# Kernel optimization log

Measured on AMD Instinct MI355X. Metric: run time of the kernel, lower is better.

## Reference

```python
import jax, jax.numpy as jnp
import numpy as np

# Standard SMPL kinematic tree (child -> parent); root's entry unused.
PARENTS = np.array([0, 0, 0, 0, 1, 2, 3, 4, 5, 6, 7, 8, 9, 9, 9, 12, 13, 14, 16, 17, 18, 19, 20, 21], dtype=np.int32)
N_JOINTS = 24


def _rodrigues(r):
    # r: [..., 3] axis-angle -> [..., 3, 3] rotation matrices.
    # Original adds N(0,1e-8) noise to avoid div-by-zero; we use a deterministic eps.
    theta = jnp.linalg.norm(r, axis=-1, keepdims=True) + 1e-8
    rh = r / theta
    cos = jnp.cos(theta)[..., None]
    sin = jnp.sin(theta)[..., None]
    z = jnp.zeros_like(rh[..., 0])
    K = jnp.stack([z, -rh[..., 2], rh[..., 1],
                   rh[..., 2], z, -rh[..., 0],
                   -rh[..., 1], rh[..., 0], z], axis=-1).reshape(r.shape[:-1] + (3, 3))
    outer = rh[..., :, None] * rh[..., None, :]
    eye = jnp.eye(3, dtype=r.dtype)
    return cos * eye + (1.0 - cos) * outer + sin * K


def setup_inputs() -> dict:
    key = jax.random.key(0)
    ks = jax.random.split(key, 7)
    N, V, J, B = 512, 6890, 24, 10
    beta = jax.random.normal(ks[0], (N, B), dtype=jnp.float32)
    pose = jax.random.normal(ks[1], (N, J * 3), dtype=jnp.float32)
    v_template = jax.random.normal(ks[2], (V, 3), dtype=jnp.float32)
    shapedirs = jax.random.normal(ks[3], (V, 3, B), dtype=jnp.float32) * 0.03
    posedirs = jax.random.normal(ks[4], (V, 3, (J - 1) * 9), dtype=jnp.float32) * 0.01
    J_regressor = jax.random.uniform(ks[5], (J, V), dtype=jnp.float32)
    J_regressor = J_regressor / jnp.sum(J_regressor, axis=1, keepdims=True)  # NonNegUnitSum(axis=1)
    weights = jax.random.uniform(ks[6], (V, J), dtype=jnp.float32)
    weights = weights / jnp.sum(weights, axis=1, keepdims=True)  # NonNegUnitSum(axis=1)
    return {"beta": beta, "pose": pose, "v_template": v_template, "shapedirs": shapedirs,
            "posedirs": posedirs, "J_regressor": J_regressor, "weights": weights}


def reference(beta, pose, v_template, shapedirs, posedirs, J_regressor, weights):
    N = beta.shape[0]
    dt = beta.dtype
    # Shape blendshapes: [N,V,3]
    v_shaped = jnp.einsum('nb,vcb->nvc', beta, shapedirs) + v_template
    # Joint locations: [N,J,3]
    J_loc = jnp.einsum('jv,nvc->njc', J_regressor, v_shaped)
    # Per-joint rotations: [N,24,3,3]
    R = _rodrigues(pose.reshape(N, N_JOINTS, 3))
    # Pose blendshapes
    lrotmin = (R[:, 1:] - jnp.eye(3, dtype=dt)).reshape(N, (N_JOINTS - 1) * 9)
    v_posed = v_shaped + jnp.einsum('np,vcp->nvc', lrotmin, posedirs)
    # Kinematic chain of 4x4 transforms
    bottom = jnp.broadcast_to(jnp.array([0.0, 0.0, 0.0, 1.0], dtype=dt), (N, 1, 4))

    def make_T(Rm, t):  # [N,3,3], [N,3] -> [N,4,4]
        return jnp.concatenate([jnp.concatenate([Rm, t[..., None]], axis=-1), bottom], axis=-2)

    G = [make_T(R[:, 0], J_loc[:, 0])]
    for i in range(1, N_JOINTS):
        p = int(PARENTS[i])
        G.append(jnp.matmul(G[p], make_T(R[:, i], J_loc[:, i] - J_loc[:, p])))
    G = jnp.stack(G, axis=1)  # [N,24,4,4]
    # Remove rest-pose joint translation: G[...,:,3] -= G @ [J,0]
    Jh = jnp.concatenate([J_loc, jnp.zeros_like(J_loc[..., :1])], axis=-1)  # [N,24,4]
    RJ = jnp.einsum('njab,njb->nja', G, Jh)
    G = G - jnp.pad(RJ[..., None], ((0, 0), (0, 0), (0, 0), (3, 0)))
    # Linear blend skinning: per-vertex blended transform [N,V,4,4]
    T = jnp.einsum('njab,vj->nvab', G, weights)
    vh = jnp.concatenate([v_posed, jnp.ones_like(v_posed[..., :1])], axis=-1)  # [N,V,4]
    v = jnp.einsum('nvab,nvb->nva', T, vh)
    return v[..., :3]
```

## Files before the change

### kernel.cpp

```cpp
#include <hip/hip_runtime.h>

#define V_CNT 6890
#define N_B 512
#define NP 207
#define RTOT 20670
#define BPACK_BLKS 1296
#define JS1_BLKS 192
#define W_BLKS 27
#define FUSE_X 108
#define FUSE_BLKS 864

typedef unsigned short ushort_t;
typedef __attribute__((ext_vector_type(4))) float f32x4;
typedef __attribute__((ext_vector_type(8))) short s16x8;
typedef __attribute__((ext_vector_type(4))) short s16x4;

#define O_PART 0u
#define O_G2   65536u
#define O_A    655360u
#define O_W    917504u
#define O_B    1441792u

__device__ __constant__ int PAR[24] = {0,0,0,0,1,2,3,4,5,6,7,8,9,9,9,12,13,14,16,17,18,19,20,21};
__device__ __constant__ int LVL[36] = {
    1, 2, 3,-1,   4, 5, 6,-1,   7, 8, 9,-1,
   10,11,12,13,  14,-1,-1,-1,  15,16,17,-1,
   18,19,-1,-1,  20,21,-1,-1,  22,23,-1,-1};

__device__ __forceinline__ ushort_t f2bf(float f) {
    union { float f; unsigned u; } x; x.f = f;
    unsigned u = x.u + 0x7fffu + ((x.u >> 16) & 1u);
    return (ushort_t)(u >> 16);
}
__device__ __forceinline__ float bf2f(ushort_t h) {
    union { unsigned u; float f; } x; x.u = ((unsigned)h) << 16;
    return x.f;
}

__global__ __launch_bounds__(256) void k_pre(const float* __restrict__ pdirs,
                                             const float* __restrict__ sdirs,
                                             const float* __restrict__ vtemp,
                                             const float* __restrict__ jreg,
                                             const float* __restrict__ wts,
                                             ushort_t* __restrict__ Bswz,
                                             float* __restrict__ part,
                                             ushort_t* __restrict__ Wp) {
    __shared__ float rows[3312];
    __shared__ float red[4][33];
    int b = blockIdx.x;
    int tid = threadIdx.x;
    if (b < BPACK_BLKS) {
        int rtile = b;
        int base = rtile * 16 * NP;
        const int TOTF = RTOT * NP;
        for (int i = tid; i < 16 * NP; i += 256) {
            int gi = base + i;
            rows[i] = (gi < TOTF) ? pdirs[gi] : 0.f;
        }
        __syncthreads();
        for (int c = tid; c < 448; c += 256) {
            int kc = c >> 6, lane = c & 63;
            int quad = lane >> 4, lm = lane & 15;
            int r = rtile * 16 + lm;
            int k0 = kc * 32 + quad * 8;
            bool rv = (r < RTOT);
            s16x8 pk;
#pragma unroll
            for (int i = 0; i < 8; i++) {
                int k = k0 + i;
                float v = 0.f;
                if (rv) {
                    if (k < NP) v = rows[lm * NP + k];
                    else if (k < 217) v = sdirs[(size_t)r * 10 + (k - NP)];
                }
                pk[i] = (short)f2bf(v);
            }
            *(s16x8*)(Bswz + ((size_t)(rtile * 7 + kc) * 64 + lane) * 8) = pk;
        }
    } else if (b < BPACK_BLKS + JS1_BLKS) {
        int b2 = b - BPACK_BLKS;
        int ch = b2 & 7;
        int j = b2 >> 3;
        int v0 = ch * 862;
        int vend = v0 + 862; if (vend > V_CNT) vend = V_CNT;
        float acc[33];
#pragma unroll
        for (int i = 0; i < 33; i++) acc[i] = 0.f;
        for (int v = v0 + tid; v < vend; v += 256) {
            float r = jreg[j * V_CNT + v];
            const float* sd = sdirs + v * 30;
#pragma unroll
            for (int i = 0; i < 30; i++) acc[i] += r * sd[i];
            acc[30] += r * vtemp[v * 3 + 0];
            acc[31] += r * vtemp[v * 3 + 1];
            acc[32] += r * vtemp[v * 3 + 2];
        }
#pragma unroll
        for (int off = 32; off > 0; off >>= 1) {
#pragma unroll
            for (int i = 0; i < 33; i++) acc[i] += __shfl_down(acc[i], off);
        }
        int w = tid >> 6, lane = tid & 63;
        if (lane == 0) {
#pragma unroll
            for (int i = 0; i < 33; i++) red[w][i] = acc[i];
        }
        __syncthreads();
        if (tid < 33) {
            float s = red[0][tid] + red[1][tid] + red[2][tid] + red[3][tid];
            part[b2 * 33 + tid] = s;
        }
    } else {
        int v = (b - BPACK_BLKS - JS1_BLKS) * 256 + tid;
        ushort_t o[32];
        if (v < V_CNT) {
            const float* wr = wts + v * 24;
#pragma unroll
            for (int j = 0; j < 24; j++) o[j] = f2bf(wr[j]);
        } else {
#pragma unroll
            for (int j = 0; j < 24; j++) o[j] = 0;
        }
#pragma unroll
        for (int j = 24; j < 32; j++) o[j] = 0;
#pragma unroll
        for (int q = 0; q < 4; q++)
            *(s16x8*)(Wp + (size_t)v * 32 + q * 8) = *(s16x8*)&o[q * 8];
    }
}

__global__ __launch_bounds__(128) void k_chain(const float* __restrict__ beta,
                                               const float* __restrict__ pose,
                                               const float* __restrict__ part,
                                               ushort_t* __restrict__ G2,
                                               ushort_t* __restrict__ Aswz) {
    __shared__ float JSl[720];
    __shared__ float JTl[72];
    __shared__ float Rl[2][24][9];
    __shared__ float Jl[2][24][3];
    __shared__ float Tm[2][24][16];
    __shared__ float G[2][24][16];
    __shared__ float Gp[2][24][12];
    int tid = threadIdx.x;

    for (int t = tid; t < 792; t += 128) {
        int j = t / 33, i = t - j * 33;
        float s = 0.f;
#pragma unroll
        for (int c = 0; c < 8; c++) s += part[(j * 8 + c) * 33 + i];
        if (i < 30) JSl[j * 30 + i] = s;
        else        JTl[j * 3 + (i - 30)] = s;
    }
    __syncthreads();

    int sub = tid >> 6, lane = tid & 63;
    int n = blockIdx.x * 2 + sub;

    if (lane < 24) {
        int t = lane;
        float x = pose[n * 72 + t * 3 + 0];
        float y = pose[n * 72 + t * 3 + 1];
        float z = pose[n * 72 + t * 3 + 2];
        float th = sqrtf(x * x + y * y + z * z) + 1e-8f;
        float inv = 1.f / th;
        float rx = x * inv, ry = y * inv, rz = z * inv;
        float c = cosf(th), s = sinf(th), omc = 1.f - c;
        Rl[sub][t][0] = c + omc * rx * rx;
        Rl[sub][t][1] = omc * rx * ry - s * rz;
        Rl[sub][t][2] = omc * rx * rz + s * ry;
        Rl[sub][t][3] = omc * ry * rx + s * rz;
        Rl[sub][t][4] = c + omc * ry * ry;
        Rl[sub][t][5] = omc * ry * rz - s * rx;
        Rl[sub][t][6] = omc * rz * rx - s * ry;
        Rl[sub][t][7] = omc * rz * ry + s * rx;
        Rl[sub][t][8] = c + omc * rz * rz;
#pragma unroll
        for (int cc = 0; cc < 3; cc++) {
            float a = JTl[t * 3 + cc];
#pragma unroll
            for (int b = 0; b < 10; b++) a += beta[n * 10 + b] * JSl[(t * 3 + cc) * 10 + b];
            Jl[sub][t][cc] = a;
        }
    }
    __syncthreads();
    if (lane < 24) {
        int t = lane;
        int p = PAR[t];
        float tx, ty, tz;
        if (t == 0) { tx = Jl[sub][0][0]; ty = Jl[sub][0][1]; tz = Jl[sub][0][2]; }
        else { tx = Jl[sub][t][0] - Jl[sub][p][0]; ty = Jl[sub][t][1] - Jl[sub][p][1]; tz = Jl[sub][t][2] - Jl[sub][p][2]; }
        Tm[sub][t][0] = Rl[sub][t][0]; Tm[sub][t][1] = Rl[sub][t][1]; Tm[sub][t][2]  = Rl[sub][t][2]; Tm[sub][t][3]  = tx;
        Tm[sub][t][4] = Rl[sub][t][3]; Tm[sub][t][5] = Rl[sub][t][4]; Tm[sub][t][6]  = Rl[sub][t][5]; Tm[sub][t][7]  = ty;
        Tm[sub][t][8] = Rl[sub][t][6]; Tm[sub][t][9] = Rl[sub][t][7]; Tm[sub][t][10] = Rl[sub][t][8]; Tm[sub][t][11] = tz;
        Tm[sub][t][12] = 0.f; Tm[sub][t][13] = 0.f; Tm[sub][t][14] = 0.f; Tm[sub][t][15] = 1.f;
    }
    __syncthreads();
    if (lane < 16) G[sub][0][lane] = Tm[sub][0][lane];
    __syncthreads();
#pragma unroll
    for (int p9 = 0; p9 < 9; p9++) {
        int slot = lane >> 4, el = lane & 15;
        int j = LVL[p9 * 4 + slot];
        if (j >= 0) {
            int par = PAR[j];
            int a = el >> 2, bb = el & 3;
            float s = G[sub][par][a * 4 + 0] * Tm[sub][j][0 * 4 + bb]
                    + G[sub][par][a * 4 + 1] * Tm[sub][j][1 * 4 + bb]
                    + G[sub][par][a * 4 + 2] * Tm[sub][j][2 * 4 + bb]
                    + G[sub][par][a * 4 + 3] * Tm[sub][j][3 * 4 + bb];
            G[sub][j][el] = s;
        }
        __syncthreads();
    }
    if (lane < 24) {
        int t = lane;
        float jx = Jl[sub][t][0], jy = Jl[sub][t][1], jz = Jl[sub][t][2];
#pragma unroll
        for (int a = 0; a < 3; a++) {
            float g0 = G[sub][t][a * 4 + 0], g1 = G[sub][t][a * 4 + 1];
            float g2 = G[sub][t][a * 4 + 2], g3 = G[sub][t][a * 4 + 3];
            Gp[sub][t][a * 4 + 0] = g0;
            Gp[sub][t][a * 4 + 1] = g1;
            Gp[sub][t][a * 4 + 2] = g2;
            Gp[sub][t][a * 4 + 3] = g3 - (g0 * jx + g1 * jy + g2 * jz);
        }
    }
    __syncthreads();
    {
        int quad = lane >> 4, lm = lane & 15;
        s16x8 pk;
#pragma unroll
        for (int jj = 0; jj < 8; jj++) {
            int joint = quad * 8 + jj;
            float val = (joint < 24 && lm < 12) ? Gp[sub][joint][lm] : 0.f;
            pk[jj] = (short)f2bf(val);
        }
        *(s16x8*)(G2 + (size_t)n * 512 + lane * 8) = pk;
    }
    if (lane < 28) {
        int kc = lane >> 2, quad2 = lane & 3;
        s16x8 pk;
#pragma unroll
        for (int j = 0; j < 8; j++) {
            int k = kc * 32 + quad2 * 8 + j;
            float val;
            if (k < NP) {
                int jo = 1 + k / 9;
                int e = k - (jo - 1) * 9;
                float d = (e == 0 || e == 4 || e == 8) ? 1.f : 0.f;
                val = Rl[sub][jo][e] - d;
            } else if (k < 217) {
                val = beta[n * 10 + (k - NP)];
            } else val = 0.f;
            pk[j] = (short)f2bf(val);
        }
        *(s16x8*)(Aswz + (((size_t)(n >> 4) * 7 + kc) * 64 + (quad2 * 16 + (n & 15))) * 8) = pk;
    }
}

__global__ __launch_bounds__(256) void k_fused(const ushort_t* __restrict__ Aswz,
                                               const ushort_t* __restrict__ Bswz,
                                               const ushort_t* __restrict__ Wp,
                                               const ushort_t* __restrict__ G2,
                                               const float* __restrict__ vtemp,
                                               float* __restrict__ out) {
    __shared__ ushort_t vp[4][96][36];
    int bid = blockIdx.x;
    int tt = (bid & 7) * FUSE_X + (bid >> 3);
    int bx = tt >> 3, by = tt & 7;
    int tid = threadIdx.x, w = tid >> 6, lane = tid & 63;
    int quad = lane >> 4, lm = lane & 15;
    int rh = w & 1, nh = w >> 1;
    int n_w = by * 64 + nh * 32;
    int vs_w = bx * 64 + rh * 32;
    int rtile0 = bx * 12 + rh * 6;
    int ntile0 = by * 4 + nh * 2;

    f32x4 acc[2][6];
#pragma unroll
    for (int a = 0; a < 2; a++)
#pragma unroll
        for (int b = 0; b < 6; b++) acc[a][b] = (f32x4)0.f;

    s16x8 af[2][2], bf[2][6];
#pragma unroll
    for (int mt = 0; mt < 2; mt++)
        af[0][mt] = *(const s16x8*)(Aswz + ((size_t)(ntile0 + mt) * 7 + 0) * 512 + lane * 8);
#pragma unroll
    for (int rt = 0; rt < 6; rt++)
        bf[0][rt] = *(const s16x8*)(Bswz + ((size_t)(rtile0 + rt) * 7 + 0) * 512 + lane * 8);
#pragma unroll
    for (int kc = 0; kc < 7; kc++) {
        int cur = kc & 1, nxt = cur ^ 1;
        if (kc < 6) {
#pragma unroll
            for (int mt = 0; mt < 2; mt++)
                af[nxt][mt] = *(const s16x8*)(Aswz + ((size_t)(ntile0 + mt) * 7 + kc + 1) * 512 + lane * 8);
#pragma unroll
            for (int rt = 0; rt < 6; rt++)
                bf[nxt][rt] = *(const s16x8*)(Bswz + ((size_t)(rtile0 + rt) * 7 + kc + 1) * 512 + lane * 8);
        }
#pragma unroll
        for (int mt = 0; mt < 2; mt++)
#pragma unroll
            for (int rt = 0; rt < 6; rt++)
                acc[mt][rt] = __builtin_amdgcn_mfma_f32_16x16x32_bf16(af[cur][mt], bf[cur][rt], acc[mt][rt], 0, 0, 0);
    }

    float vt[6];
#pragma unroll
    for (int rt = 0; rt < 6; rt++) {
        int col = bx * 192 + rh * 96 + rt * 16 + lm;
        vt[rt] = (col < RTOT) ? vtemp[col] : 0.f;
    }
#pragma unroll
    for (int mt = 0; mt < 2; mt++) {
#pragma unroll
        for (int rt = 0; rt < 6; rt++) {
            int rl = rt * 16 + lm;
            int nl0 = mt * 16 + quad * 4;
            s16x4 pk;
            pk[0] = (short)f2bf(acc[mt][rt][0] + vt[rt]);
            pk[1] = (short)f2bf(acc[mt][rt][1] + vt[rt]);
            pk[2] = (short)f2bf(acc[mt][rt][2] + vt[rt]);
            pk[3] = (short)f2bf(acc[mt][rt][3] + vt[rt]);
            *(s16x4*)&vp[w][rl][nl0] = pk;
        }
    }

    s16x8 wf[2];
#pragma unroll
    for (int mt = 0; mt < 2; mt++)
        wf[mt] = *(const s16x8*)(Wp + (size_t)(vs_w + mt * 16 + lm) * 32 + quad * 8);

    s16x8 ga = *(const s16x8*)(G2 + (size_t)n_w * 512 + lane * 8);
    s16x8 gb = *(const s16x8*)(G2 + (size_t)(n_w + 1) * 512 + lane * 8);
#pragma unroll 1
    for (int t = 0; t < 16; t++) {
        int na = n_w + 2 * t;
        s16x8 gan, gbn;
        if (t < 15) {
            gan = *(const s16x8*)(G2 + (size_t)(na + 2) * 512 + lane * 8);
            gbn = *(const s16x8*)(G2 + (size_t)(na + 3) * 512 + lane * 8);
        }
        f32x4 ta[2], tb[2];
#pragma unroll
        for (int mt = 0; mt < 2; mt++) {
            ta[mt] = __builtin_amdgcn_mfma_f32_16x16x32_bf16(ga, wf[mt], (f32x4)0.f, 0, 0, 0);
            tb[mt] = __builtin_amdgcn_mfma_f32_16x16x32_bf16(gb, wf[mt], (f32x4)0.f, 0, 0, 0);
        }
        if (quad < 3) {
#pragma unroll
            for (int mt = 0; mt < 2; mt++) {
                int v = vs_w + mt * 16 + lm;
                if (v < V_CNT) {
                    int vloc = mt * 16 + lm;
                    unsigned pw0 = *(const unsigned*)&vp[w][vloc * 3 + 0][2 * t];
                    unsigned pw1 = *(const unsigned*)&vp[w][vloc * 3 + 1][2 * t];
                    unsigned pw2 = *(const unsigned*)&vp[w][vloc * 3 + 2][2 * t];
                    float p0a = bf2f((ushort_t)(pw0 & 0xffffu)), p0b = bf2f((ushort_t)(pw0 >> 16));
                    float p1a = bf2f((ushort_t)(pw1 & 0xffffu)), p1b = bf2f((ushort_t)(pw1 >> 16));
                    float p2a = bf2f((ushort_t)(pw2 & 0xffffu)), p2b = bf2f((ushort_t)(pw2 >> 16));
                    float oa = ta[mt][3] + ta[mt][0] * p0a + ta[mt][1] * p1a + ta[mt][2] * p2a;
                    float ob = tb[mt][3] + tb[mt][0] * p0b + tb[mt][1] * p1b + tb[mt][2] * p2b;
                    out[((size_t)na * V_CNT + v) * 3 + quad] = oa;
                    out[((size_t)(na + 1) * V_CNT + v) * 3 + quad] = ob;
                }
            }
        }
        ga = gan; gb = gbn;
    }
}

extern "C" void kernel_launch(void* const* d_in, const int* in_sizes, int n_in,
                              void* d_out, int out_size, void* d_ws, size_t ws_size,
                              hipStream_t stream) {
    const float* beta  = (const float*)d_in[0];
    const float* pose  = (const float*)d_in[1];
    const float* vtemp = (const float*)d_in[2];
    const float* sdirs = (const float*)d_in[3];
    const float* pdirs = (const float*)d_in[4];
    const float* jreg  = (const float*)d_in[5];
    const float* wts   = (const float*)d_in[6];
    char* ws = (char*)d_ws;
    float*    ws_part = (float*)(ws + O_PART);
    ushort_t* ws_G2   = (ushort_t*)(ws + O_G2);
    ushort_t* ws_A    = (ushort_t*)(ws + O_A);
    ushort_t* ws_W    = (ushort_t*)(ws + O_W);
    ushort_t* ws_B    = (ushort_t*)(ws + O_B);
    float* out = (float*)d_out;

    k_pre<<<dim3(BPACK_BLKS + JS1_BLKS + W_BLKS), dim3(256), 0, stream>>>(
        pdirs, sdirs, vtemp, jreg, wts, ws_B, ws_part, ws_W);
    k_chain<<<dim3(N_B / 2), dim3(128), 0, stream>>>(beta, pose, ws_part, ws_G2, ws_A);
    k_fused<<<dim3(FUSE_BLKS), dim3(256), 0, stream>>>(ws_A, ws_B, ws_W, ws_G2, vtemp, out);
}
```

Measured before the change: 128.9 us.

## Regroup prep kernels so chain overlaps B-pack, unroll skinning loop by four

The joint-regressor reduction now runs as its own small first kernel. The kinematic-chain work, 4 poses per 256-thread block, is merged into the same launch as the posedirs bf16 packing and weight packing. This lets the serial chain stage overlap the bandwidth-heavy packing instead of running after it. Separately, the skinning loop in the fused kernel now processes four poses per iteration with prefetched G2 fragments, aiming for more MFMA and memory-level parallelism at the cost of extra registers.

After: 125.1 us. 1.03x faster.

```diff
diff --git a/kernel.cpp b/kernel.cpp
--- a/kernel.cpp
+++ b/kernel.cpp
@@ -4,9 +4,11 @@
 #define N_B 512
 #define NP 207
 #define RTOT 20670
+#define CHAIN_BLKS 128
 #define BPACK_BLKS 1296
+#define W_BLKS 27
+#define PREP_BLKS (CHAIN_BLKS + BPACK_BLKS + W_BLKS)
 #define JS1_BLKS 192
-#define W_BLKS 27
 #define FUSE_X 108
 #define FUSE_BLKS 864
 
@@ -37,20 +39,186 @@
     return x.f;
 }
 
-__global__ __launch_bounds__(256) void k_pre(const float* __restrict__ pdirs,
-                                             const float* __restrict__ sdirs,
-                                             const float* __restrict__ vtemp,
-                                             const float* __restrict__ jreg,
-                                             const float* __restrict__ wts,
-                                             ushort_t* __restrict__ Bswz,
-                                             float* __restrict__ part,
-                                             ushort_t* __restrict__ Wp) {
-    __shared__ float rows[3312];
+__global__ __launch_bounds__(256) void k_js(const float* __restrict__ jreg,
+                                            const float* __restrict__ sdirs,
+                                            const float* __restrict__ vtemp,
+                                            float* __restrict__ part) {
     __shared__ float red[4][33];
+    int b2 = blockIdx.x;
+    int tid = threadIdx.x;
+    int ch = b2 & 7;
+    int j = b2 >> 3;
+    int v0 = ch * 862;
+    int vend = v0 + 862; if (vend > V_CNT) vend = V_CNT;
+    float acc[33];
+#pragma unroll
+    for (int i = 0; i < 33; i++) acc[i] = 0.f;
+    for (int v = v0 + tid; v < vend; v += 256) {
+        float r = jreg[j * V_CNT + v];
+        const float* sd = sdirs + v * 30;
+#pragma unroll
+        for (int i = 0; i < 30; i++) acc[i] += r * sd[i];
+        acc[30] += r * vtemp[v * 3 + 0];
+        acc[31] += r * vtemp[v * 3 + 1];
+        acc[32] += r * vtemp[v * 3 + 2];
+    }
+#pragma unroll
+    for (int off = 32; off > 0; off >>= 1) {
+#pragma unroll
+        for (int i = 0; i < 33; i++) acc[i] += __shfl_down(acc[i], off);
+    }
+    int w = tid >> 6, lane = tid & 63;
+    if (lane == 0) {
+#pragma unroll
+        for (int i = 0; i < 33; i++) red[w][i] = acc[i];
+    }
+    __syncthreads();
+    if (tid < 33) {
+        float s = red[0][tid] + red[1][tid] + red[2][tid] + red[3][tid];
+        part[b2 * 33 + tid] = s;
+    }
+}
+
+__global__ __launch_bounds__(256) void k_prep(const float* __restrict__ beta,
+                                              const float* __restrict__ pose,
+                                              const float* __restrict__ part,
+                                              const float* __restrict__ pdirs,
+                                              const float* __restrict__ sdirs,
+                                              const float* __restrict__ wts,
+                                              ushort_t* __restrict__ G2,
+                                              ushort_t* __restrict__ Aswz,
+                                              ushort_t* __restrict__ Bswz,
+                                              ushort_t* __restrict__ Wp) {
+    __shared__ __align__(16) char smem[24672];
     int b = blockIdx.x;
     int tid = threadIdx.x;
-    if (b < BPACK_BLKS) {
-        int rtile = b;
+
+    if (b < CHAIN_BLKS) {
+        float* smem_f = (float*)smem;
+        float* JSl = smem_f;
+        float* JTl = smem_f + 720;
+        float (*Rl)[24][9]  = (float (*)[24][9])(smem_f + 792);
+        float (*Jl)[24][3]  = (float (*)[24][3])(smem_f + 1656);
+        float (*Tm)[24][16] = (float (*)[24][16])(smem_f + 1944);
+        float (*G )[24][16] = (float (*)[24][16])(smem_f + 3480);
+        float (*Gp)[24][12] = (float (*)[24][12])(smem_f + 5016);
+
+        for (int t = tid; t < 792; t += 256) {
+            int j = t / 33, i = t - j * 33;
+            float s = 0.f;
+#pragma unroll
+            for (int c = 0; c < 8; c++) s += part[(j * 8 + c) * 33 + i];
+            if (i < 30) JSl[j * 30 + i] = s;
+            else        JTl[j * 3 + (i - 30)] = s;
+        }
+        __syncthreads();
+
+        int sub = tid >> 6, lane = tid & 63;
+        int n = b * 4 + sub;
+
+        if (lane < 24) {
+            int t = lane;
+            float x = pose[n * 72 + t * 3 + 0];
+            float y = pose[n * 72 + t * 3 + 1];
+            float z = pose[n * 72 + t * 3 + 2];
+            float th = sqrtf(x * x + y * y + z * z) + 1e-8f;
+            float inv = 1.f / th;
+            float rx = x * inv, ry = y * inv, rz = z * inv;
+            float c = cosf(th), s = sinf(th), omc = 1.f - c;
+            Rl[sub][t][0] = c + omc * rx * rx;
+            Rl[sub][t][1] = omc * rx * ry - s * rz;
+            Rl[sub][t][2] = omc * rx * rz + s * ry;
+            Rl[sub][t][3] = omc * ry * rx + s * rz;
+            Rl[sub][t][4] = c + omc * ry * ry;
+            Rl[sub][t][5] = omc * ry * rz - s * rx;
+            Rl[sub][t][6] = omc * rz * rx - s * ry;
+            Rl[sub][t][7] = omc * rz * ry + s * rx;
+            Rl[sub][t][8] = c + omc * rz * rz;
+#pragma unroll
+            for (int cc = 0; cc < 3; cc++) {
+                float a = JTl[t * 3 + cc];
+#pragma unroll
+                for (int bb = 0; bb < 10; bb++) a += beta[n * 10 + bb] * JSl[(t * 3 + cc) * 10 + bb];
+                Jl[sub][t][cc] = a;
+            }
+        }
+        __syncthreads();
+        if (lane < 24) {
+            int t = lane;
+            int p = PAR[t];
+            float tx, ty, tz;
+            if (t == 0) { tx = Jl[sub][0][0]; ty = Jl[sub][0][1]; tz = Jl[sub][0][2]; }
+            else { tx = Jl[sub][t][0] - Jl[sub][p][0]; ty = Jl[sub][t][1] - Jl[sub][p][1]; tz = Jl[sub][t][2] - Jl[sub][p][2]; }
+            Tm[sub][t][0] = Rl[sub][t][0]; Tm[sub][t][1] = Rl[sub][t][1]; Tm[sub][t][2]  = Rl[sub][t][2]; Tm[sub][t][3]  = tx;
+            Tm[sub][t][4] = Rl[sub][t][3]; Tm[sub][t][5] = Rl[sub][t][4]; Tm[sub][t][6]  = Rl[sub][t][5]; Tm[sub][t][7]  = ty;
+            Tm[sub][t][8] = Rl[sub][t][6]; Tm[sub][t][9] = Rl[sub][t][7]; Tm[sub][t][10] = Rl[sub][t][8]; Tm[sub][t][11] = tz;
+            Tm[sub][t][12] = 0.f; Tm[sub][t][13] = 0.f; Tm[sub][t][14] = 0.f; Tm[sub][t][15] = 1.f;
+        }
+        __syncthreads();
+        if (lane < 16) G[sub][0][lane] = Tm[sub][0][lane];
+        __syncthreads();
+#pragma unroll
+        for (int p9 = 0; p9 < 9; p9++) {
+            int slot = lane >> 4, el = lane & 15;
+            int j = LVL[p9 * 4 + slot];
+            if (j >= 0) {
+                int par = PAR[j];
+                int a = el >> 2, bb = el & 3;
+                float s = G[sub][par][a * 4 + 0] * Tm[sub][j][0 * 4 + bb]
+                        + G[sub][par][a * 4 + 1] * Tm[sub][j][1 * 4 + bb]
+                        + G[sub][par][a * 4 + 2] * Tm[sub][j][2 * 4 + bb]
+                        + G[sub][par][a * 4 + 3] * Tm[sub][j][3 * 4 + bb];
+                G[sub][j][el] = s;
+            }
+            __syncthreads();
+        }
+        if (lane < 24) {
+            int t = lane;
+            float jx = Jl[sub][t][0], jy = Jl[sub][t][1], jz = Jl[sub][t][2];
+#pragma unroll
+            for (int a = 0; a < 3; a++) {
+                float g0 = G[sub][t][a * 4 + 0], g1 = G[sub][t][a * 4 + 1];
+                float g2 = G[sub][t][a * 4 + 2], g3 = G[sub][t][a * 4 + 3];
+                Gp[sub][t][a * 4 + 0] = g0;
+                Gp[sub][t][a * 4 + 1] = g1;
+                Gp[sub][t][a * 4 + 2] = g2;
+                Gp[sub][t][a * 4 + 3] = g3 - (g0 * jx + g1 * jy + g2 * jz);
+            }
+        }
+        __syncthreads();
+        {
+            int quad = lane >> 4, lm = lane & 15;
+            s16x8 pk;
+#pragma unroll
+            for (int jj = 0; jj < 8; jj++) {
+                int joint = quad * 8 + jj;
+                float val = (joint < 24 && lm < 12) ? Gp[sub][joint][lm] : 0.f;
+                pk[jj] = (short)f2bf(val);
+            }
+            *(s16x8*)(G2 + (size_t)n * 512 + lane * 8) = pk;
+        }
+        if (lane < 28) {
+            int kc = lane >> 2, quad2 = lane & 3;
+            s16x8 pk;
+#pragma unroll
+            for (int j = 0; j < 8; j++) {
+                int k = kc * 32 + quad2 * 8 + j;
+                float val;
+                if (k < NP) {
+                    int jo = 1 + k / 9;
+                    int e = k - (jo - 1) * 9;
+                    float d = (e == 0 || e == 4 || e == 8) ? 1.f : 0.f;
+                    val = Rl[sub][jo][e] - d;
+                } else if (k < 217) {
+                    val = beta[n * 10 + (k - NP)];
+                } else val = 0.f;
+                pk[j] = (short)f2bf(val);
+            }
+            *(s16x8*)(Aswz + (((size_t)(n >> 4) * 7 + kc) * 64 + (quad2 * 16 + (n & 15))) * 8) = pk;
+        }
+    } else if (b < CHAIN_BLKS + BPACK_BLKS) {
+        float* rows = (float*)smem;
+        int rtile = b - CHAIN_BLKS;
         int base = rtile * 16 * NP;
         const int TOTF = RTOT * NP;
         for (int i = tid; i < 16 * NP; i += 256) {
@@ -77,41 +245,8 @@
             }
             *(s16x8*)(Bswz + ((size_t)(rtile * 7 + kc) * 64 + lane) * 8) = pk;
         }
-    } else if (b < BPACK_BLKS + JS1_BLKS) {
-        int b2 = b - BPACK_BLKS;
-        int ch = b2 & 7;
-        int j = b2 >> 3;
-        int v0 = ch * 862;
-        int vend = v0 + 862; if (vend > V_CNT) vend = V_CNT;
-        float acc[33];
-#pragma unroll
-        for (int i = 0; i < 33; i++) acc[i] = 0.f;
-        for (int v = v0 + tid; v < vend; v += 256) {
-            float r = jreg[j * V_CNT + v];
-            const float* sd = sdirs + v * 30;
-#pragma unroll
-            for (int i = 0; i < 30; i++) acc[i] += r * sd[i];
-            acc[30] += r * vtemp[v * 3 + 0];
-            acc[31] += r * vtemp[v * 3 + 1];
-            acc[32] += r * vtemp[v * 3 + 2];
-        }
-#pragma unroll
-        for (int off = 32; off > 0; off >>= 1) {
-#pragma unroll
-            for (int i = 0; i < 33; i++) acc[i] += __shfl_down(acc[i], off);
-        }
-        int w = tid >> 6, lane = tid & 63;
-        if (lane == 0) {
-#pragma unroll
-            for (int i = 0; i < 33; i++) red[w][i] = acc[i];
-        }
-        __syncthreads();
-        if (tid < 33) {
-            float s = red[0][tid] + red[1][tid] + red[2][tid] + red[3][tid];
-            part[b2 * 33 + tid] = s;
-        }
     } else {
-        int v = (b - BPACK_BLKS - JS1_BLKS) * 256 + tid;
+        int v = (b - CHAIN_BLKS - BPACK_BLKS) * 256 + tid;
         ushort_t o[32];
         if (v < V_CNT) {
             const float* wr = wts + v * 24;
@@ -126,135 +261,6 @@
 #pragma unroll
         for (int q = 0; q < 4; q++)
             *(s16x8*)(Wp + (size_t)v * 32 + q * 8) = *(s16x8*)&o[q * 8];
-    }
-}
-
-__global__ __launch_bounds__(128) void k_chain(const float* __restrict__ beta,
-                                               const float* __restrict__ pose,
-                                               const float* __restrict__ part,
-                                               ushort_t* __restrict__ G2,
-                                               ushort_t* __restrict__ Aswz) {
-    __shared__ float JSl[720];
-    __shared__ float JTl[72];
-    __shared__ float Rl[2][24][9];
-    __shared__ float Jl[2][24][3];
-    __shared__ float Tm[2][24][16];
-    __shared__ float G[2][24][16];
-    __shared__ float Gp[2][24][12];
-    int tid = threadIdx.x;
-
-    for (int t = tid; t < 792; t += 128) {
-        int j = t / 33, i = t - j * 33;
-        float s = 0.f;
-#pragma unroll
-        for (int c = 0; c < 8; c++) s += part[(j * 8 + c) * 33 + i];
-        if (i < 30) JSl[j * 30 + i] = s;
-        else        JTl[j * 3 + (i - 30)] = s;
-    }
-    __syncthreads();
-
-    int sub = tid >> 6, lane = tid & 63;
-    int n = blockIdx.x * 2 + sub;
-
-    if (lane < 24) {
-        int t = lane;
-        float x = pose[n * 72 + t * 3 + 0];
-        float y = pose[n * 72 + t * 3 + 1];
-        float z = pose[n * 72 + t * 3 + 2];
-        float th = sqrtf(x * x + y * y + z * z) + 1e-8f;
-        float inv = 1.f / th;
-        float rx = x * inv, ry = y * inv, rz = z * inv;
-        float c = cosf(th), s = sinf(th), omc = 1.f - c;
-        Rl[sub][t][0] = c + omc * rx * rx;
-        Rl[sub][t][1] = omc * rx * ry - s * rz;
-        Rl[sub][t][2] = omc * rx * rz + s * ry;
-        Rl[sub][t][3] = omc * ry * rx + s * rz;
-        Rl[sub][t][4] = c + omc * ry * ry;
-        Rl[sub][t][5] = omc * ry * rz - s * rx;
-        Rl[sub][t][6] = omc * rz * rx - s * ry;
-        Rl[sub][t][7] = omc * rz * ry + s * rx;
-        Rl[sub][t][8] = c + omc * rz * rz;
-#pragma unroll
-        for (int cc = 0; cc < 3; cc++) {
-            float a = JTl[t * 3 + cc];
-#pragma unroll
-            for (int b = 0; b < 10; b++) a += beta[n * 10 + b] * JSl[(t * 3 + cc) * 10 + b];
-            Jl[sub][t][cc] = a;
-        }
-    }
-    __syncthreads();
-    if (lane < 24) {
-        int t = lane;
-        int p = PAR[t];
-        float tx, ty, tz;
-        if (t == 0) { tx = Jl[sub][0][0]; ty = Jl[sub][0][1]; tz = Jl[sub][0][2]; }
-        else { tx = Jl[sub][t][0] - Jl[sub][p][0]; ty = Jl[sub][t][1] - Jl[sub][p][1]; tz = Jl[sub][t][2] - Jl[sub][p][2]; }
-        Tm[sub][t][0] = Rl[sub][t][0]; Tm[sub][t][1] = Rl[sub][t][1]; Tm[sub][t][2]  = Rl[sub][t][2]; Tm[sub][t][3]  = tx;
-        Tm[sub][t][4] = Rl[sub][t][3]; Tm[sub][t][5] = Rl[sub][t][4]; Tm[sub][t][6]  = Rl[sub][t][5]; Tm[sub][t][7]  = ty;
-        Tm[sub][t][8] = Rl[sub][t][6]; Tm[sub][t][9] = Rl[sub][t][7]; Tm[sub][t][10] = Rl[sub][t][8]; Tm[sub][t][11] = tz;
-        Tm[sub][t][12] = 0.f; Tm[sub][t][13] = 0.f; Tm[sub][t][14] = 0.f; Tm[sub][t][15] = 1.f;
-    }
-    __syncthreads();
-    if (lane < 16) G[sub][0][lane] = Tm[sub][0][lane];
-    __syncthreads();
-#pragma unroll
-    for (int p9 = 0; p9 < 9; p9++) {
-        int slot = lane >> 4, el = lane & 15;
-        int j = LVL[p9 * 4 + slot];
-        if (j >= 0) {
-            int par = PAR[j];
-            int a = el >> 2, bb = el & 3;
-            float s = G[sub][par][a * 4 + 0] * Tm[sub][j][0 * 4 + bb]
-                    + G[sub][par][a * 4 + 1] * Tm[sub][j][1 * 4 + bb]
-                    + G[sub][par][a * 4 + 2] * Tm[sub][j][2 * 4 + bb]
-                    + G[sub][par][a * 4 + 3] * Tm[sub][j][3 * 4 + bb];
-            G[sub][j][el] = s;
-        }
-        __syncthreads();
-    }
-    if (lane < 24) {
-        int t = lane;
-        float jx = Jl[sub][t][0], jy = Jl[sub][t][1], jz = Jl[sub][t][2];
-#pragma unroll
-        for (int a = 0; a < 3; a++) {
-            float g0 = G[sub][t][a * 4 + 0], g1 = G[sub][t][a * 4 + 1];
-            float g2 = G[sub][t][a * 4 + 2], g3 = G[sub][t][a * 4 + 3];
-            Gp[sub][t][a * 4 + 0] = g0;
-            Gp[sub][t][a * 4 + 1] = g1;
-            Gp[sub][t][a * 4 + 2] = g2;
-            Gp[sub][t][a * 4 + 3] = g3 - (g0 * jx + g1 * jy + g2 * jz);
-        }
-    }
-    __syncthreads();
-    {
-        int quad = lane >> 4, lm = lane & 15;
-        s16x8 pk;
-#pragma unroll
-        for (int jj = 0; jj < 8; jj++) {
-            int joint = quad * 8 + jj;
-            float val = (joint < 24 && lm < 12) ? Gp[sub][joint][lm] : 0.f;
-            pk[jj] = (short)f2bf(val);
-        }
-        *(s16x8*)(G2 + (size_t)n * 512 + lane * 8) = pk;
-    }
-    if (lane < 28) {
-        int kc = lane >> 2, quad2 = lane & 3;
-        s16x8 pk;
-#pragma unroll
-        for (int j = 0; j < 8; j++) {
-            int k = kc * 32 + quad2 * 8 + j;
-            float val;
-            if (k < NP) {
-                int jo = 1 + k / 9;
-                int e = k - (jo - 1) * 9;
-                float d = (e == 0 || e == 4 || e == 8) ? 1.f : 0.f;
-                val = Rl[sub][jo][e] - d;
-            } else if (k < 217) {
-                val = beta[n * 10 + (k - NP)];
-            } else val = 0.f;
-            pk[j] = (short)f2bf(val);
-        }
-        *(s16x8*)(Aswz + (((size_t)(n >> 4) * 7 + kc) * 64 + (quad2 * 16 + (n & 15))) * 8) = pk;
     }
 }
 
@@ -333,31 +339,35 @@
     for (int mt = 0; mt < 2; mt++)
         wf[mt] = *(const s16x8*)(Wp + (size_t)(vs_w + mt * 16 + lm) * 32 + quad * 8);
 
-    s16x8 ga = *(const s16x8*)(G2 + (size_t)n_w * 512 + lane * 8);
-    s16x8 gb = *(const s16x8*)(G2 + (size_t)(n_w + 1) * 512 + lane * 8);
+#define LDG2(nn) (*(const s16x8*)(G2 + (size_t)(nn) * 512 + lane * 8))
+    s16x8 gaE = LDG2(n_w + 0), gbE = LDG2(n_w + 1);
+    s16x8 gaO = LDG2(n_w + 2), gbO = LDG2(n_w + 3);
 #pragma unroll 1
-    for (int t = 0; t < 16; t++) {
-        int na = n_w + 2 * t;
-        s16x8 gan, gbn;
-        if (t < 15) {
-            gan = *(const s16x8*)(G2 + (size_t)(na + 2) * 512 + lane * 8);
-            gbn = *(const s16x8*)(G2 + (size_t)(na + 3) * 512 + lane * 8);
-        }
-        f32x4 ta[2], tb[2];
+    for (int t2 = 0; t2 < 8; t2++) {
+        int na = n_w + 4 * t2;
+        s16x8 nE0, nE1, nO0, nO1;
+        if (t2 < 7) {
+            nE0 = LDG2(na + 4); nE1 = LDG2(na + 5);
+            nO0 = LDG2(na + 6); nO1 = LDG2(na + 7);
+        }
+        f32x4 ta[2], tb[2], tc[2], td[2];
 #pragma unroll
         for (int mt = 0; mt < 2; mt++) {
-            ta[mt] = __builtin_amdgcn_mfma_f32_16x16x32_bf16(ga, wf[mt], (f32x4)0.f, 0, 0, 0);
-            tb[mt] = __builtin_amdgcn_mfma_f32_16x16x32_bf16(gb, wf[mt], (f32x4)0.f, 0, 0, 0);
+            ta[mt] = __builtin_amdgcn_mfma_f32_16x16x32_bf16(gaE, wf[mt], (f32x4)0.f, 0, 0, 0);
+            tb[mt] = __builtin_amdgcn_mfma_f32_16x16x32_bf16(gbE, wf[mt], (f32x4)0.f, 0, 0, 0);
+            tc[mt] = __builtin_amdgcn_mfma_f32_16x16x32_bf16(gaO, wf[mt], (f32x4)0.f, 0, 0, 0);
+            td[mt] = __builtin_amdgcn_mfma_f32_16x16x32_bf16(gbO, wf[mt], (f32x4)0.f, 0, 0, 0);
         }
         if (quad < 3) {
+            int c0 = 4 * t2;
 #pragma unroll
             for (int mt = 0; mt < 2; mt++) {
                 int v = vs_w + mt * 16 + lm;
                 if (v < V_CNT) {
                     int vloc = mt * 16 + lm;
-                    unsigned pw0 = *(const unsigned*)&vp[w][vloc * 3 + 0][2 * t];
-                    unsigned pw1 = *(const unsigned*)&vp[w][vloc * 3 + 1][2 * t];
-                    unsigned pw2 = *(const unsigned*)&vp[w][vloc * 3 + 2][2 * t];
+                    unsigned pw0 = *(const unsigned*)&vp[w][vloc * 3 + 0][c0];
+                    unsigned pw1 = *(const unsigned*)&vp[w][vloc * 3 + 1][c0];
+                    unsigned pw2 = *(const unsigned*)&vp[w][vloc * 3 + 2][c0];
                     float p0a = bf2f((ushort_t)(pw0 & 0xffffu)), p0b = bf2f((ushort_t)(pw0 >> 16));
                     float p1a = bf2f((ushort_t)(pw1 & 0xffffu)), p1b = bf2f((ushort_t)(pw1 >> 16));
                     float p2a = bf2f((ushort_t)(pw2 & 0xffffu)), p2b = bf2f((ushort_t)(pw2 >> 16));
@@ -365,11 +375,22 @@
                     float ob = tb[mt][3] + tb[mt][0] * p0b + tb[mt][1] * p1b + tb[mt][2] * p2b;
                     out[((size_t)na * V_CNT + v) * 3 + quad] = oa;
                     out[((size_t)(na + 1) * V_CNT + v) * 3 + quad] = ob;
+                    unsigned qw0 = *(const unsigned*)&vp[w][vloc * 3 + 0][c0 + 2];
+                    unsigned qw1 = *(const unsigned*)&vp[w][vloc * 3 + 1][c0 + 2];
+                    unsigned qw2 = *(const unsigned*)&vp[w][vloc * 3 + 2][c0 + 2];
+                    float q0a = bf2f((ushort_t)(qw0 & 0xffffu)), q0b = bf2f((ushort_t)(qw0 >> 16));
+                    float q1a = bf2f((ushort_t)(qw1 & 0xffffu)), q1b = bf2f((ushort_t)(qw1 >> 16));
+                    float q2a = bf2f((ushort_t)(qw2 & 0xffffu)), q2b = bf2f((ushort_t)(qw2 >> 16));
+                    float oc = tc[mt][3] + tc[mt][0] * q0a + tc[mt][1] * q1a + tc[mt][2] * q2a;
+                    float od = td[mt][3] + td[mt][0] * q0b + td[mt][1] * q1b + td[mt][2] * q2b;
+                    out[((size_t)(na + 2) * V_CNT + v) * 3 + quad] = oc;
+                    out[((size_t)(na + 3) * V_CNT + v) * 3 + quad] = od;
                 }
             }
         }
-        ga = gan; gb = gbn;
-    }
+        gaE = nE0; gbE = nE1; gaO = nO0; gbO = nO1;
+    }
+#undef LDG2
 }
 
 extern "C" void kernel_launch(void* const* d_in, const int* in_sizes, int n_in,
@@ -390,8 +411,8 @@
     ushort_t* ws_B    = (ushort_t*)(ws + O_B);
     float* out = (float*)d_out;
 
-    k_pre<<<dim3(BPACK_BLKS + JS1_BLKS + W_BLKS), dim3(256), 0, stream>>>(
-        pdirs, sdirs, vtemp, jreg, wts, ws_B, ws_part, ws_W);
-    k_chain<<<dim3(N_B / 2), dim3(128), 0, stream>>>(beta, pose, ws_part, ws_G2, ws_A);
+    k_js<<<dim3(JS1_BLKS), dim3(256), 0, stream>>>(jreg, sdirs, vtemp, ws_part);
+    k_prep<<<dim3(PREP_BLKS), dim3(256), 0, stream>>>(
+        beta, pose, ws_part, pdirs, sdirs, wts, ws_G2, ws_A, ws_B, ws_W);
     k_fused<<<dim3(FUSE_BLKS), dim3(256), 0, stream>>>(ws_A, ws_B, ws_W, ws_G2, vtemp, out);
 }
```
